# Performance work log

Hardware: AMD Instinct MI355X
Metric: run time of the kernel (lower is better)

The kernel has to match this reference:

```python
import jax, jax.numpy as jnp
import numpy as np

B, R, K, D = 65536, 8, 8, 256


def setup_inputs() -> dict:
    key = jax.random.key(0)
    ks = jax.random.split(key, 7)
    return {
        "fine_memory": jax.random.normal(ks[0], (B, R, D), dtype=jnp.float32),
        "compressed_memory": jax.random.normal(ks[1], (B, K, D), dtype=jnp.float32),
        "fm_count": jax.random.randint(ks[2], (B,), 0, R + 1),
        "new_segment": jax.random.normal(ks[3], (B, D), dtype=jnp.float32),
        "valid_mask": jax.random.randint(ks[4], (B,), 0, 2).astype(bool),
        "conv_w": jax.random.normal(ks[5], (D, D, 2), dtype=jnp.float32) * 0.05,
        "conv_b": jax.random.normal(ks[6], (D,), dtype=jnp.float32) * 0.05,
    }


def reference(fine_memory, compressed_memory, fm_count, new_segment, valid_mask, conv_w, conv_b):
    """Vectorized CompressiveMemory.update().

    Per sample b (only where valid_mask[b]):
      - if fm_count[b] < R: write new_segment into fm slot fm_count[b]; count += 1
      - else: c_new = Conv1d([cm_last, fm_oldest]); shift cm left, append c_new;
              shift fm left, append new_segment.
    """
    b, r, d = fine_memory.shape
    insert = valid_mask & (fm_count < r)          # (B,) append into free slot
    shift = valid_mask & (fm_count >= r)          # (B,) FIFO shift + compress

    # --- insert branch: masked one-hot scatter of new_segment at position fm_count
    onehot = (jnp.arange(r)[None, :] == fm_count[:, None]) & insert[:, None]  # (B,R)
    fm_ins = jnp.where(onehot[:, :, None], new_segment[:, None, :], fine_memory)

    # --- shift branch: compress [cm_last, fm_oldest] with 2-tap conv (out,in,k)
    c_new = (jnp.einsum('bi,oi->bo', compressed_memory[:, -1], conv_w[:, :, 0])
             + jnp.einsum('bi,oi->bo', fine_memory[:, 0], conv_w[:, :, 1])
             + conv_b)  # (B,D)
    cm_shift = jnp.concatenate([compressed_memory[:, 1:], c_new[:, None, :]], axis=1)
    fm_shift = jnp.concatenate([fine_memory[:, 1:], new_segment[:, None, :]], axis=1)

    fm_new = jnp.where(shift[:, None, None], fm_shift, fm_ins)
    cm_new = jnp.where(shift[:, None, None], cm_shift, compressed_memory)
    fm_count_new = fm_count + insert.astype(fm_count.dtype)
    return fm_new, cm_new, fm_count_new
```

## Files before the change

kernel.cpp:

```cpp
#include <hip/hip_runtime.h>


#define NB 65536
#define RR 8
#define KK 8
#define DD 256
#define WFLOATS (DD * DD * 2)

#define WS_LIST_OFF 64
#define WS_WT_OFF   (64 + NB * 4)

__global__ __launch_bounds__(256) void transpose_w(
    const float* __restrict__ W, float* __restrict__ Wt)
{
    int t = blockIdx.x * 256 + threadIdx.x;
    int o = t >> 9;
    int m = t & 511;
    Wt[m * DD + o] = W[t];
}

__global__ __launch_bounds__(256) void stream_update(
    const float* __restrict__ fm,
    const float* __restrict__ cm,
    const int* __restrict__ cnt_in,
    const float* __restrict__ seg,
    const int* __restrict__ valid,
    float* __restrict__ out_fm,
    float* __restrict__ out_cm,
    float* __restrict__ out_cnt,
    int* __restrict__ counter,
    int* __restrict__ list)
{
    const int row  = blockIdx.x * 4 + (threadIdx.x >> 6);
    const int lane = threadIdx.x & 63;
    const int b    = row >> 4;
    const int sub  = row & 15;
    const int c    = lane << 2;

    const int  cnt = cnt_in[b];
    const bool v   = valid[b] != 0;
    const bool ins = v && (cnt < RR);
    const bool shf = v && (cnt >= RR);

    if (sub < 8) {
        const float* src;
        if (shf)      src = (sub < 7) ? fm + ((size_t)b * RR + sub + 1) * DD
                                      : seg + (size_t)b * DD;
        else if (ins && sub == cnt)
                      src = seg + (size_t)b * DD;
        else          src = fm + ((size_t)b * RR + sub) * DD;
        float4 x = *(const float4*)(src + c);
        *(float4*)(out_fm + ((size_t)b * RR + sub) * DD + c) = x;

        if (sub == 0 && lane == 0) {
            out_cnt[b] = (float)(cnt + (ins ? 1 : 0));
            if (shf) { int p = atomicAdd(counter, 1); list[p] = b; }
        }
    } else {
        const int j = sub - 8;
        if (shf) {
            if (j < 7) {
                float4 x = *(const float4*)(cm + ((size_t)b * KK + j + 1) * DD + c);
                *(float4*)(out_cm + ((size_t)b * KK + j) * DD + c) = x;
            }
        } else {
            float4 x = *(const float4*)(cm + ((size_t)b * KK + j) * DD + c);
            *(float4*)(out_cm + ((size_t)b * KK + j) * DD + c) = x;
        }
    }
}

#define SPB 32
#define SPW 8

__global__ __launch_bounds__(256) void conv_kernel(
    const float* __restrict__ fm,
    const float* __restrict__ cm,
    const float* __restrict__ Wt,
    const float* __restrict__ bias,
    float* __restrict__ out_cm,
    const int* __restrict__ counter,
    const int* __restrict__ list)
{
    __shared__ float xbuf[SPB][512];
    const int count = *counter;
    const int base  = blockIdx.x * SPB;
    if (base >= count) return;

    const int wave = threadIdx.x >> 6;
    const int lane = threadIdx.x & 63;
    const int s0   = wave * SPW;

    int bs[SPW];
    #pragma unroll
    for (int s = 0; s < SPW; ++s) {
        const int idx = base + s0 + s;
        bs[s] = (idx < count) ? list[idx] : -1;
        if (bs[s] >= 0) {
            const float* cl = cm + ((size_t)bs[s] * KK + (KK - 1)) * DD;
            const float* f0 = fm + (size_t)bs[s] * RR * DD;
            float4 cv = *(const float4*)(cl + lane * 4);
            float4 fv = *(const float4*)(f0 + lane * 4);
            *(float4*)&xbuf[s0 + s][lane * 8]     = make_float4(cv.x, fv.x, cv.y, fv.y);
            *(float4*)&xbuf[s0 + s][lane * 8 + 4] = make_float4(cv.z, fv.z, cv.w, fv.w);
        }
    }

    float acc[SPW][4];
    #pragma unroll
    for (int s = 0; s < SPW; ++s)
        acc[s][0] = acc[s][1] = acc[s][2] = acc[s][3] = 0.f;

    for (int m4 = 0; m4 < 128; ++m4) {
        const float4 w0 = *(const float4*)(Wt + (size_t)(m4 * 4 + 0) * DD + lane * 4);
        const float4 w1 = *(const float4*)(Wt + (size_t)(m4 * 4 + 1) * DD + lane * 4);
        const float4 w2 = *(const float4*)(Wt + (size_t)(m4 * 4 + 2) * DD + lane * 4);
        const float4 w3 = *(const float4*)(Wt + (size_t)(m4 * 4 + 3) * DD + lane * 4);
        #pragma unroll
        for (int s = 0; s < SPW; ++s) {
            const float4 xq = *(const float4*)&xbuf[s0 + s][m4 * 4];
            acc[s][0] += xq.x * w0.x + xq.y * w1.x + xq.z * w2.x + xq.w * w3.x;
            acc[s][1] += xq.x * w0.y + xq.y * w1.y + xq.z * w2.y + xq.w * w3.y;
            acc[s][2] += xq.x * w0.z + xq.y * w1.z + xq.z * w2.z + xq.w * w3.z;
            acc[s][3] += xq.x * w0.w + xq.y * w1.w + xq.z * w2.w + xq.w * w3.w;
        }
    }

    const float4 bv = *(const float4*)(bias + lane * 4);
    #pragma unroll
    for (int s = 0; s < SPW; ++s) {
        if (bs[s] >= 0) {
            float4 r = make_float4(acc[s][0] + bv.x, acc[s][1] + bv.y,
                                   acc[s][2] + bv.z, acc[s][3] + bv.w);
            *(float4*)(out_cm + ((size_t)bs[s] * KK + (KK - 1)) * DD + lane * 4) = r;
        }
    }
}

extern "C" void kernel_launch(void* const* d_in, const int* in_sizes, int n_in,
                              void* d_out, int out_size, void* d_ws, size_t ws_size,
                              hipStream_t stream) {
    const float* fm    = (const float*)d_in[0];
    const float* cm    = (const float*)d_in[1];
    const int*   cnt   = (const int*)d_in[2];
    const float* seg   = (const float*)d_in[3];
    const int*   valid = (const int*)d_in[4];
    const float* W     = (const float*)d_in[5];
    const float* bias  = (const float*)d_in[6];

    float* out_fm  = (float*)d_out;
    float* out_cm  = out_fm + (size_t)NB * RR * DD;
    float* out_cnt = out_cm + (size_t)NB * KK * DD;

    int*   counter = (int*)d_ws;
    int*   list    = (int*)((char*)d_ws + WS_LIST_OFF);
    float* Wt      = (float*)((char*)d_ws + WS_WT_OFF);

    hipMemsetAsync(d_ws, 0, 64, stream);

    hipLaunchKernelGGL(transpose_w, dim3(WFLOATS / 256), dim3(256), 0, stream, W, Wt);
    hipLaunchKernelGGL(stream_update, dim3(NB * 16 / 4), dim3(256), 0, stream,
                       fm, cm, cnt, seg, valid, out_fm, out_cm, out_cnt, counter, list);
    hipLaunchKernelGGL(conv_kernel, dim3(NB / SPB), dim3(256), 0, stream,
                       fm, cm, Wt, bias, out_cm, counter, list);
}
```

Baseline: 458.4 us.

## Use one block per sample with nontemporal copies and fold counter reset into transpose

The streaming update kernel now assigns one 256-thread block per sample, each wave copying two fm rows and two cm rows, instead of one wave per row over 16 rows. Loads and stores use nontemporal builtins so the large one-pass copy does not pollute the cache. The memset of the counter is removed and the counter is zeroed inside the transpose kernel, dropping one stream operation. The trade-off is fewer blocks, each doing more work, and fm rows read again by the conv kernel may now miss in cache.

```diff
diff --git a/kernel.cpp b/kernel.cpp
--- a/kernel.cpp
+++ b/kernel.cpp
@@ -10,10 +10,20 @@
 #define WS_LIST_OFF 64
 #define WS_WT_OFF   (64 + NB * 4)
 
+typedef float f4 __attribute__((ext_vector_type(4)));
+
+static __device__ __forceinline__ f4 ntload(const float* p) {
+    return __builtin_nontemporal_load((const f4*)p);
+}
+static __device__ __forceinline__ void ntstore(float* p, f4 v) {
+    __builtin_nontemporal_store(v, (f4*)p);
+}
+
 __global__ __launch_bounds__(256) void transpose_w(
-    const float* __restrict__ W, float* __restrict__ Wt)
+    const float* __restrict__ W, float* __restrict__ Wt, int* __restrict__ counter)
 {
     int t = blockIdx.x * 256 + threadIdx.x;
+    if (t == 0) *counter = 0;
     int o = t >> 9;
     int m = t & 511;
     Wt[m * DD + o] = W[t];
@@ -31,10 +41,9 @@
     int* __restrict__ counter,
     int* __restrict__ list)
 {
-    const int row  = blockIdx.x * 4 + (threadIdx.x >> 6);
+    const int b    = blockIdx.x;
+    const int w    = threadIdx.x >> 6;
     const int lane = threadIdx.x & 63;
-    const int b    = row >> 4;
-    const int sub  = row & 15;
     const int c    = lane << 2;
 
     const int  cnt = cnt_in[b];
@@ -42,31 +51,35 @@
     const bool ins = v && (cnt < RR);
     const bool shf = v && (cnt >= RR);
 
-    if (sub < 8) {
-        const float* src;
-        if (shf)      src = (sub < 7) ? fm + ((size_t)b * RR + sub + 1) * DD
-                                      : seg + (size_t)b * DD;
-        else if (ins && sub == cnt)
-                      src = seg + (size_t)b * DD;
-        else          src = fm + ((size_t)b * RR + sub) * DD;
-        float4 x = *(const float4*)(src + c);
-        *(float4*)(out_fm + ((size_t)b * RR + sub) * DD + c) = x;
+    const float* fmb  = fm  + (size_t)b * (RR * DD);
+    const float* cmb  = cm  + (size_t)b * (KK * DD);
+    const float* segb = seg + (size_t)b * DD;
+    float* ofm = out_fm + (size_t)b * (RR * DD);
+    float* ocm = out_cm + (size_t)b * (KK * DD);
 
-        if (sub == 0 && lane == 0) {
-            out_cnt[b] = (float)(cnt + (ins ? 1 : 0));
-            if (shf) { int p = atomicAdd(counter, 1); list[p] = b; }
-        }
-    } else {
-        const int j = sub - 8;
-        if (shf) {
-            if (j < 7) {
-                float4 x = *(const float4*)(cm + ((size_t)b * KK + j + 1) * DD + c);
-                *(float4*)(out_cm + ((size_t)b * KK + j) * DD + c) = x;
-            }
-        } else {
-            float4 x = *(const float4*)(cm + ((size_t)b * KK + j) * DD + c);
-            *(float4*)(out_cm + ((size_t)b * KK + j) * DD + c) = x;
-        }
+    const int r0 = w, r1 = w + 4;
+
+    const float* f0src = shf ? fmb + (r0 + 1) * DD
+                             : (ins && r0 == cnt) ? segb : fmb + r0 * DD;
+    const float* f1src = shf ? ((r1 < 7) ? fmb + (r1 + 1) * DD : segb)
+                             : (ins && r1 == cnt) ? segb : fmb + r1 * DD;
+    const bool   c1st  = !(shf && r1 == 7);
+    const float* c0src = cmb + (shf ? r0 + 1 : r0) * DD;
+    const float* c1src = c1st ? cmb + (shf ? r1 + 1 : r1) * DD : cmb;
+
+    f4 a = ntload(f0src + c);
+    f4 bq = ntload(f1src + c);
+    f4 d = ntload(c0src + c);
+    f4 e = ntload(c1src + c);
+
+    ntstore(ofm + r0 * DD + c, a);
+    ntstore(ofm + r1 * DD + c, bq);
+    ntstore(ocm + r0 * DD + c, d);
+    if (c1st) ntstore(ocm + r1 * DD + c, e);
+
+    if (w == 0 && lane == 0) {
+        out_cnt[b] = (float)(cnt + (ins ? 1 : 0));
+        if (shf) { int p = atomicAdd(counter, 1); list[p] = b; }
     }
 }
 
@@ -156,10 +169,8 @@
     int*   list    = (int*)((char*)d_ws + WS_LIST_OFF);
     float* Wt      = (float*)((char*)d_ws + WS_WT_OFF);
 
-    hipMemsetAsync(d_ws, 0, 64, stream);
-
-    hipLaunchKernelGGL(transpose_w, dim3(WFLOATS / 256), dim3(256), 0, stream, W, Wt);
-    hipLaunchKernelGGL(stream_update, dim3(NB * 16 / 4), dim3(256), 0, stream,
+    hipLaunchKernelGGL(transpose_w, dim3(WFLOATS / 256), dim3(256), 0, stream, W, Wt, counter);
+    hipLaunchKernelGGL(stream_update, dim3(NB), dim3(256), 0, stream,
                        fm, cm, cnt, seg, valid, out_fm, out_cm, out_cnt, counter, list);
     hipLaunchKernelGGL(conv_kernel, dim3(NB / SPB), dim3(256), 0, stream,
                        fm, cm, Wt, bias, out_cm, counter, list);
```

Result: faster. 434.7 us (-5.2%).
